# Performance work log

Measured on AMD Instinct MI355X. Metric: run time of the kernel, lower is better.

The kernel has to match this reference:

```python
import jax, jax.numpy as jnp
import numpy as np

B = 65536
R = 160            # radial_len (capped at MAX_RADIAL_LEN)
EDGE_SINK_WIDTH = 8


def setup_inputs() -> dict:
    key = jax.random.key(0)
    k1, k2 = jax.random.split(key)
    return {
        "history": jax.random.uniform(k1, (B, R, 3), dtype=jnp.float32),
        "color_rgb": jax.random.uniform(k2, (B, 3), dtype=jnp.float32),
        "offset_per_frame_60hz": jnp.float32(1.3),
        "persistence_per_frame_60hz": jnp.float32(0.92),
        "diffusion01": jnp.float32(0.5),
        "dt_seconds": jnp.float32(1.0 / 60.0),
        "amount01": jnp.float32(0.8),
        "spread01": jnp.float32(0.4),
    }


def _forward(history, color_rgb, offset, persistence, diffusion01, dt_seconds, amount01, spread01):
    dt = jnp.clip(dt_seconds, 0.0, 0.05)
    dt_scale = dt * 60.0
    dt_offset = offset * dt_scale
    dt_persist = persistence ** dt_scale

    # ---- inject at centre: 5-bin spread kernel, then clamp to [0,1] ----
    amount = jnp.clip(amount01, 0.0, 1.0)
    spread = jnp.clip(spread01, 0.0, 1.0)
    energy = color_rgb * amount                      # [B,3]
    tight = 1.0 - spread
    w = jnp.stack([0.5 + 0.4 * tight,
                   0.2 * spread + 0.05,
                   0.12 * spread,
                   0.06 * spread,
                   0.02 * spread])                   # [5]
    h = history.at[:, :5, :].add(energy[:, None, :] * w[None, :, None])
    h = jnp.clip(h, 0.0, 1.0)

    # ---- semi-Lagrangian push advection (vectorized scatter-add) ----
    i = jnp.arange(R, dtype=h.dtype)                 # source bin positions
    new_pos = i + dt_offset
    valid = (new_pos >= 0.0) & (new_pos < R - 1)     # bins outside are dropped
    left = jnp.clip(jnp.floor(new_pos).astype(jnp.int32), 0, R - 2)
    frac = new_pos - left.astype(h.dtype)
    wl = jnp.where(valid, (1.0 - frac) * dt_persist, 0.0)  # [R]
    wr = jnp.where(valid, frac * dt_persist, 0.0)
    work = jnp.zeros_like(h)
    work = work.at[:, left, :].add(h * wl[None, :, None])
    work = work.at[:, left + 1, :].add(h * wr[None, :, None])
    h = work

    # ---- diffusion: [k, 1-2k, k] stencil with ZERO boundary taps ----
    k = 0.15 * diffusion01
    c = 1.0 - 2.0 * k
    padded = jnp.pad(h, ((0, 0), (1, 1), (0, 0)))    # zero pad matches torch boundary
    h = c * h + k * padded[:, :-2, :] + k * padded[:, 2:, :]

    # ---- quadratic edge sink over last EDGE_SINK_WIDTH bins ----
    idx = jnp.arange(R)
    t = (R - 1 - idx).astype(h.dtype) / float(EDGE_SINK_WIDTH)
    fade = jnp.where(idx >= R - EDGE_SINK_WIDTH, t * t, jnp.ones((), h.dtype))
    h = h * fade[None, :, None]
    return h


def reference(history, color_rgb, offset_per_frame_60hz, persistence_per_frame_60hz,
              diffusion01, dt_seconds, amount01, spread01):
    return _forward(history, color_rgb, offset_per_frame_60hz,
                    persistence_per_frame_60hz, diffusion01, dt_seconds,
                    amount01, spread01)
```

## Files before the change

### kernel.cpp

```cpp
#include <hip/hip_runtime.h>
#include <math.h>

#define RBINS 160
#define BROWS 65536
#define ROWELEMS 480
#define ROWF4 (ROWELEMS / 4)
#define TASKS_PER_ROW 40
#define NTHREADS 256
#define TOTAL_TASKS (BROWS * TASKS_PER_ROW)
#define NBLOCKS (TOTAL_TASKS / NTHREADS)

__device__ __forceinline__ float clamp01(float x) {
    return __builtin_amdgcn_fmed3f(x, 0.0f, 1.0f);
}

template<int P>
__device__ __forceinline__ void stencil_store(
    const float* __restrict__ w,
    float u1, float u2, float u3, float u4,
    float4* __restrict__ dst, bool dofade, int j0)
{
    float r[12];
    #pragma unroll
    for (int m = 0; m < 12; ++m) {
        float acc = u1 * w[P + m];
        acc = fmaf(u2, w[P + m + 3], acc);
        acc = fmaf(u3, w[P + m + 6], acc);
        acc = fmaf(u4, w[P + m + 9], acc);
        r[m] = acc;
    }
    if (dofade) {
        #pragma unroll
        for (int mb = 0; mb < 4; ++mb) {
            const int j = j0 + mb;
            const float t = (float)(RBINS - 1 - j) * 0.125f;
            const float ff = (j >= RBINS - 8) ? t * t : 1.0f;
            r[3*mb+0] *= ff; r[3*mb+1] *= ff; r[3*mb+2] *= ff;
        }
    }
    dst[0] = make_float4(r[0], r[1], r[2],  r[3]);
    dst[1] = make_float4(r[4], r[5], r[6],  r[7]);
    dst[2] = make_float4(r[8], r[9], r[10], r[11]);
}

__global__ __launch_bounds__(NTHREADS, 6) void beat_kernel(
    const float* __restrict__ hist,
    const float* __restrict__ color,
    const float* __restrict__ p_offset,
    const float* __restrict__ p_persist,
    const float* __restrict__ p_diff,
    const float* __restrict__ p_dt,
    const float* __restrict__ p_amount,
    const float* __restrict__ p_spread,
    float* __restrict__ out)
{
    const int task = blockIdx.x * NTHREADS + threadIdx.x;
    const int b = task / TASKS_PER_ROW;
    const int c = task - b * TASKS_PER_ROW;

    const float offs = *p_offset;
    const float pers = *p_persist;
    const float diff = *p_diff;
    const float dts  = *p_dt;

    const float dt       = fminf(fmaxf(dts, 0.0f), 0.05f);
    const float dt_scale = dt * 60.0f;
    const float s        = offs * dt_scale;
    const float dt_pers  = __powf(pers, dt_scale);
    const int   dfl      = (int)floorf(s);
    const float frac     = s - (float)dfl;
    const float kk = 0.15f * diff;
    const float cc = 1.0f - 2.0f * kk;
    const float wl = (1.0f - frac) * dt_pers;
    const float wr = frac * dt_pers;
    const float u1 = wr * kk;
    const float u2 = fmaf(wl, kk, wr * cc);
    const float u3 = fmaf(wl, cc, wr * kk);
    const float u4 = wl * kk;

    const int ilo = max(0, (int)ceilf(-s));
    const int ihi = min(RBINS - 1, (int)ceilf((float)(RBINS - 1) - s) - 1);
    const int flo = 3 * ilo;
    const int fhi = 3 * ihi + 3;

    const int e0 = c * 12;
    const int A  = e0 - 6 - 3 * dfl;
    const int p  = A & 3;
    const int a0 = A - p;

    const float4* src4 = (const float4*)hist + (size_t)b * ROWF4;
    float w[24];
    #pragma unroll
    for (int q = 0; q < 6; ++q) {
        int idx = (a0 >> 2) + q;
        idx = min(max(idx, 0), ROWF4 - 1);
        const float4 v = src4[idx];
        w[4*q+0] = v.x; w[4*q+1] = v.y; w[4*q+2] = v.z; w[4*q+3] = v.w;
    }

    if (a0 < 15) {
        const float am = fminf(fmaxf(*p_amount, 0.0f), 1.0f);
        const float sp = fminf(fmaxf(*p_spread, 0.0f), 1.0f);
        const float tight = 1.0f - sp;
        const float aw0 = am * fmaf(0.4f, tight, 0.5f);
        const float aw1 = am * fmaf(0.2f, sp, 0.05f);
        const float aw2 = am * (0.12f * sp);
        const float aw3 = am * (0.06f * sp);
        const float aw4 = am * (0.02f * sp);
        const float c0 = color[3*b+0];
        const float c1 = color[3*b+1];
        const float c2 = color[3*b+2];
        #pragma unroll
        for (int u = 0; u < 24; ++u) {
            const int f = a0 + u;
            if ((unsigned)f < 15u) {
                const int bin = f / 3;
                const int ch  = f - 3 * bin;
                const float cv = (ch == 0) ? c0 : (ch == 1) ? c1 : c2;
                const float av = (bin == 0) ? aw0 : (bin == 1) ? aw1 :
                                 (bin == 2) ? aw2 : (bin == 3) ? aw3 : aw4;
                w[u] += cv * av;
            }
        }
    }

    #pragma unroll
    for (int u = 0; u < 24; ++u) {
        const int f = a0 + u;
        const bool m = (f >= flo) && (f < fhi);
        w[u] = m ? clamp01(w[u]) : 0.0f;
    }

    float4* dst = (float4*)(out + (size_t)b * ROWELEMS + e0);
    const bool dofade = (c >= TASKS_PER_ROW - 2);
    const int j0 = 4 * c;
    switch (p) {
        case 0:  stencil_store<0>(w, u1, u2, u3, u4, dst, dofade, j0); break;
        case 1:  stencil_store<1>(w, u1, u2, u3, u4, dst, dofade, j0); break;
        case 2:  stencil_store<2>(w, u1, u2, u3, u4, dst, dofade, j0); break;
        default: stencil_store<3>(w, u1, u2, u3, u4, dst, dofade, j0); break;
    }
}

extern "C" void kernel_launch(void* const* d_in, const int* in_sizes, int n_in,
                              void* d_out, int out_size, void* d_ws, size_t ws_size,
                              hipStream_t stream) {
    const float* hist      = (const float*)d_in[0];
    const float* color     = (const float*)d_in[1];
    const float* p_offset  = (const float*)d_in[2];
    const float* p_persist = (const float*)d_in[3];
    const float* p_diff    = (const float*)d_in[4];
    const float* p_dt      = (const float*)d_in[5];
    const float* p_amount  = (const float*)d_in[6];
    const float* p_spread  = (const float*)d_in[7];
    float* outp = (float*)d_out;

    beat_kernel<<<dim3(NBLOCKS), dim3(NTHREADS), 0, stream>>>(
        hist, color, p_offset, p_persist, p_diff, p_dt, p_amount, p_spread, outp);
}
```

Measured before the change: 230.8 us.

## Split inject-region tasks into separate fixup blocks to remove divergent inject path

Main blocks now return early for tasks near the row start that need the centre injection, and 512 extra blocks handle those tasks in a grid-stride loop. This keeps the injection branch and the color loads out of the hot main path, and occupancy bounds are raised from 6 to 8. The cost is extra blocks that partly idle, because fix threads compute but only store when A<15, plus more branching code and register pressure.

```diff
diff --git a/kernel.cpp b/kernel.cpp
--- a/kernel.cpp
+++ b/kernel.cpp
@@ -7,20 +7,22 @@
 #define ROWF4 (ROWELEMS / 4)
 #define TASKS_PER_ROW 40
 #define NTHREADS 256
-#define TOTAL_TASKS (BROWS * TASKS_PER_ROW)
-#define NBLOCKS (TOTAL_TASKS / NTHREADS)
+#define NBLOCKS_MAIN ((BROWS * TASKS_PER_ROW) / NTHREADS)
+#define CFIX 8
+#define NBLOCKS_FIX 512
+#define FIXTHREADS (NBLOCKS_FIX * NTHREADS)
+#define FIXITERS ((BROWS * CFIX) / FIXTHREADS)
 
 __device__ __forceinline__ float clamp01(float x) {
     return __builtin_amdgcn_fmed3f(x, 0.0f, 1.0f);
 }
 
 template<int P>
-__device__ __forceinline__ void stencil_store(
+__device__ __forceinline__ void stencil12(
     const float* __restrict__ w,
     float u1, float u2, float u3, float u4,
-    float4* __restrict__ dst, bool dofade, int j0)
+    float* __restrict__ r)
 {
-    float r[12];
     #pragma unroll
     for (int m = 0; m < 12; ++m) {
         float acc = u1 * w[P + m];
@@ -29,21 +31,31 @@
         acc = fmaf(u4, w[P + m + 9], acc);
         r[m] = acc;
     }
-    if (dofade) {
-        #pragma unroll
-        for (int mb = 0; mb < 4; ++mb) {
-            const int j = j0 + mb;
-            const float t = (float)(RBINS - 1 - j) * 0.125f;
-            const float ff = (j >= RBINS - 8) ? t * t : 1.0f;
-            r[3*mb+0] *= ff; r[3*mb+1] *= ff; r[3*mb+2] *= ff;
+}
+
+__device__ __forceinline__ void inject24(
+    float* __restrict__ w, int a0,
+    const float* __restrict__ color, int b,
+    float aw0, float aw1, float aw2, float aw3, float aw4)
+{
+    const float c0 = color[3*b+0];
+    const float c1 = color[3*b+1];
+    const float c2 = color[3*b+2];
+    #pragma unroll
+    for (int u = 0; u < 24; ++u) {
+        const int f = a0 + u;
+        if ((unsigned)f < 15u) {
+            const int bin = f / 3;
+            const int ch  = f - 3 * bin;
+            const float cv = (ch == 0) ? c0 : (ch == 1) ? c1 : c2;
+            const float av = (bin == 0) ? aw0 : (bin == 1) ? aw1 :
+                             (bin == 2) ? aw2 : (bin == 3) ? aw3 : aw4;
+            w[u] += cv * av;
         }
     }
-    dst[0] = make_float4(r[0], r[1], r[2],  r[3]);
-    dst[1] = make_float4(r[4], r[5], r[6],  r[7]);
-    dst[2] = make_float4(r[8], r[9], r[10], r[11]);
-}
-
-__global__ __launch_bounds__(NTHREADS, 6) void beat_kernel(
+}
+
+__global__ __launch_bounds__(NTHREADS, 8) void beat_kernel(
     const float* __restrict__ hist,
     const float* __restrict__ color,
     const float* __restrict__ p_offset,
@@ -54,10 +66,6 @@
     const float* __restrict__ p_spread,
     float* __restrict__ out)
 {
-    const int task = blockIdx.x * NTHREADS + threadIdx.x;
-    const int b = task / TASKS_PER_ROW;
-    const int c = task - b * TASKS_PER_ROW;
-
     const float offs = *p_offset;
     const float pers = *p_persist;
     const float diff = *p_diff;
@@ -83,22 +91,69 @@
     const int flo = 3 * ilo;
     const int fhi = 3 * ihi + 3;
 
-    const int e0 = c * 12;
-    const int A  = e0 - 6 - 3 * dfl;
-    const int p  = A & 3;
-    const int a0 = A - p;
-
-    const float4* src4 = (const float4*)hist + (size_t)b * ROWF4;
-    float w[24];
-    #pragma unroll
-    for (int q = 0; q < 6; ++q) {
-        int idx = (a0 >> 2) + q;
-        idx = min(max(idx, 0), ROWF4 - 1);
-        const float4 v = src4[idx];
-        w[4*q+0] = v.x; w[4*q+1] = v.y; w[4*q+2] = v.z; w[4*q+3] = v.w;
-    }
-
-    if (a0 < 15) {
+    if (blockIdx.x < NBLOCKS_MAIN) {
+        const int task = blockIdx.x * NTHREADS + threadIdx.x;
+        const int b = task / TASKS_PER_ROW;
+        const int c = task - b * TASKS_PER_ROW;
+        const int e0 = c * 12;
+        const int A  = e0 - 6 - 3 * dfl;
+        const int p  = A & 3;
+        const int a0 = A - p;
+        if (A < 15 && c < CFIX) return;
+
+        const float4* src4 = (const float4*)hist + (size_t)b * ROWF4;
+        float w[24];
+        const int q0 = a0 >> 2;
+        #pragma unroll
+        for (int q = 0; q < 6; ++q) {
+            const int idx = min(max(q0 + q, 0), ROWF4 - 1);
+            const float4 v = src4[idx];
+            w[4*q+0] = v.x; w[4*q+1] = v.y; w[4*q+2] = v.z; w[4*q+3] = v.w;
+        }
+
+        if (A < 15) {
+            const float am = fminf(fmaxf(*p_amount, 0.0f), 1.0f);
+            const float sp = fminf(fmaxf(*p_spread, 0.0f), 1.0f);
+            const float tight = 1.0f - sp;
+            inject24(w, a0, color, b,
+                     am * fmaf(0.4f, tight, 0.5f), am * fmaf(0.2f, sp, 0.05f),
+                     am * (0.12f * sp), am * (0.06f * sp), am * (0.02f * sp));
+        }
+
+        const int lo_u = flo - a0;
+        const int hi_u = fhi - a0;
+        #pragma unroll
+        for (int u = 0; u < 24; ++u) {
+            const bool v = (u >= lo_u) && (u < hi_u);
+            w[u] = v ? clamp01(w[u]) : 0.0f;
+        }
+
+        float r[12];
+        switch (p) {
+            case 0:  stencil12<0>(w, u1, u2, u3, u4, r); break;
+            case 1:  stencil12<1>(w, u1, u2, u3, u4, r); break;
+            case 2:  stencil12<2>(w, u1, u2, u3, u4, r); break;
+            default: stencil12<3>(w, u1, u2, u3, u4, r); break;
+        }
+
+        if (c >= TASKS_PER_ROW - 2) {
+            const int j0 = 4 * c;
+            #pragma unroll
+            for (int mb = 0; mb < 4; ++mb) {
+                const int j = j0 + mb;
+                const float t = (float)(RBINS - 1 - j) * 0.125f;
+                const float ff = (j >= RBINS - 8) ? t * t : 1.0f;
+                r[3*mb+0] *= ff; r[3*mb+1] *= ff; r[3*mb+2] *= ff;
+            }
+        }
+
+        float4* dst = (float4*)(out + (size_t)b * ROWELEMS + e0);
+        dst[0] = make_float4(r[0], r[1], r[2],  r[3]);
+        dst[1] = make_float4(r[4], r[5], r[6],  r[7]);
+        dst[2] = make_float4(r[8], r[9], r[10], r[11]);
+    } else {
+        const int fixtid = (blockIdx.x - NBLOCKS_MAIN) * NTHREADS + threadIdx.x;
+
         const float am = fminf(fmaxf(*p_amount, 0.0f), 1.0f);
         const float sp = fminf(fmaxf(*p_spread, 0.0f), 1.0f);
         const float tight = 1.0f - sp;
@@ -107,38 +162,53 @@
         const float aw2 = am * (0.12f * sp);
         const float aw3 = am * (0.06f * sp);
         const float aw4 = am * (0.02f * sp);
-        const float c0 = color[3*b+0];
-        const float c1 = color[3*b+1];
-        const float c2 = color[3*b+2];
-        #pragma unroll
-        for (int u = 0; u < 24; ++u) {
-            const int f = a0 + u;
-            if ((unsigned)f < 15u) {
-                const int bin = f / 3;
-                const int ch  = f - 3 * bin;
-                const float cv = (ch == 0) ? c0 : (ch == 1) ? c1 : c2;
-                const float av = (bin == 0) ? aw0 : (bin == 1) ? aw1 :
-                                 (bin == 2) ? aw2 : (bin == 3) ? aw3 : aw4;
-                w[u] += cv * av;
-            }
-        }
-    }
-
-    #pragma unroll
-    for (int u = 0; u < 24; ++u) {
-        const int f = a0 + u;
-        const bool m = (f >= flo) && (f < fhi);
-        w[u] = m ? clamp01(w[u]) : 0.0f;
-    }
-
-    float4* dst = (float4*)(out + (size_t)b * ROWELEMS + e0);
-    const bool dofade = (c >= TASKS_PER_ROW - 2);
-    const int j0 = 4 * c;
-    switch (p) {
-        case 0:  stencil_store<0>(w, u1, u2, u3, u4, dst, dofade, j0); break;
-        case 1:  stencil_store<1>(w, u1, u2, u3, u4, dst, dofade, j0); break;
-        case 2:  stencil_store<2>(w, u1, u2, u3, u4, dst, dofade, j0); break;
-        default: stencil_store<3>(w, u1, u2, u3, u4, dst, dofade, j0); break;
+
+        #pragma unroll 1
+        for (int k = 0; k < FIXITERS; ++k) {
+            const int t = fixtid + k * FIXTHREADS;
+            const int b = t >> 3;
+            const int c = t & (CFIX - 1);
+            const int e0 = c * 12;
+            const int A  = e0 - 6 - 3 * dfl;
+            const int p  = A & 3;
+            const int a0 = A - p;
+
+            const float4* src4 = (const float4*)hist + (size_t)b * ROWF4;
+            float w[24];
+            const int q0 = a0 >> 2;
+            #pragma unroll
+            for (int q = 0; q < 6; ++q) {
+                const int idx = min(max(q0 + q, 0), ROWF4 - 1);
+                const float4 v = src4[idx];
+                w[4*q+0] = v.x; w[4*q+1] = v.y; w[4*q+2] = v.z; w[4*q+3] = v.w;
+            }
+
+            if (A < 15)
+                inject24(w, a0, color, b, aw0, aw1, aw2, aw3, aw4);
+
+            const int lo_u = flo - a0;
+            const int hi_u = fhi - a0;
+            #pragma unroll
+            for (int u = 0; u < 24; ++u) {
+                const bool v = (u >= lo_u) && (u < hi_u);
+                w[u] = v ? clamp01(w[u]) : 0.0f;
+            }
+
+            float r[12];
+            switch (p) {
+                case 0:  stencil12<0>(w, u1, u2, u3, u4, r); break;
+                case 1:  stencil12<1>(w, u1, u2, u3, u4, r); break;
+                case 2:  stencil12<2>(w, u1, u2, u3, u4, r); break;
+                default: stencil12<3>(w, u1, u2, u3, u4, r); break;
+            }
+
+            if (A < 15) {
+                float4* dst = (float4*)(out + (size_t)b * ROWELEMS + e0);
+                dst[0] = make_float4(r[0], r[1], r[2],  r[3]);
+                dst[1] = make_float4(r[4], r[5], r[6],  r[7]);
+                dst[2] = make_float4(r[8], r[9], r[10], r[11]);
+            }
+        }
     }
 }
 
@@ -155,6 +225,6 @@
     const float* p_spread  = (const float*)d_in[7];
     float* outp = (float*)d_out;
 
-    beat_kernel<<<dim3(NBLOCKS), dim3(NTHREADS), 0, stream>>>(
+    beat_kernel<<<dim3(NBLOCKS_MAIN + NBLOCKS_FIX), dim3(NTHREADS), 0, stream>>>(
         hist, color, p_offset, p_persist, p_diff, p_dt, p_amount, p_spread, outp);
 }
```

New measurement: 271.4 us. +17.6%, slower.

## Double per-thread output tile, split injection rows into separate fix blocks

Applied to the files above, without the earlier changes.

Each thread now produces 24 output floats (8 bins) instead of 12, loading 9 float4s instead of 6, which cuts the redundant halo loads per output. Threads in the first chunk that need the centre injection return early, and a separate set of blocks handles those rows so the main blocks avoid the divergent injection path. Stores become nontemporal, and the launch bound drops to 4 waves per SIMD to make room for the larger register tile. The risks are lower occupancy and an extra tail of fix blocks.

```diff
diff --git a/kernel.cpp b/kernel.cpp
--- a/kernel.cpp
+++ b/kernel.cpp
@@ -5,45 +5,98 @@
 #define BROWS 65536
 #define ROWELEMS 480
 #define ROWF4 (ROWELEMS / 4)
-#define TASKS_PER_ROW 40
+#define TASKS_PER_ROW 20
 #define NTHREADS 256
-#define TOTAL_TASKS (BROWS * TASKS_PER_ROW)
-#define NBLOCKS (TOTAL_TASKS / NTHREADS)
+#define NBLOCKS_MAIN ((BROWS * TASKS_PER_ROW) / NTHREADS)
+#define NBLOCKS_FIX (BROWS / NTHREADS)
+
+typedef float f32x4 __attribute__((ext_vector_type(4)));
 
 __device__ __forceinline__ float clamp01(float x) {
     return __builtin_amdgcn_fmed3f(x, 0.0f, 1.0f);
 }
 
-template<int P>
-__device__ __forceinline__ void stencil_store(
+__device__ __forceinline__ void nt_store4(float* p, float a, float b, float c, float d) {
+    f32x4 v = {a, b, c, d};
+    __builtin_nontemporal_store(v, (f32x4*)p);
+}
+
+template<int P, int H>
+__device__ __forceinline__ void stencil_half(
     const float* __restrict__ w,
     float u1, float u2, float u3, float u4,
-    float4* __restrict__ dst, bool dofade, int j0)
-{
-    float r[12];
+    float* __restrict__ r)
+{
     #pragma unroll
     for (int m = 0; m < 12; ++m) {
-        float acc = u1 * w[P + m];
-        acc = fmaf(u2, w[P + m + 3], acc);
-        acc = fmaf(u3, w[P + m + 6], acc);
-        acc = fmaf(u4, w[P + m + 9], acc);
+        const int base = P + 12 * H + m;
+        float acc = u1 * w[base];
+        acc = fmaf(u2, w[base + 3], acc);
+        acc = fmaf(u3, w[base + 6], acc);
+        acc = fmaf(u4, w[base + 9], acc);
         r[m] = acc;
     }
-    if (dofade) {
+}
+
+template<int P>
+__device__ __forceinline__ void compute_store24(
+    const float* __restrict__ w,
+    float u1, float u2, float u3, float u4,
+    float* __restrict__ outp, bool fadeq, int bin0)
+{
+    float r[12];
+    stencil_half<P, 0>(w, u1, u2, u3, u4, r);
+    if (fadeq) {
         #pragma unroll
         for (int mb = 0; mb < 4; ++mb) {
-            const int j = j0 + mb;
+            const int j = bin0 + mb;
             const float t = (float)(RBINS - 1 - j) * 0.125f;
             const float ff = (j >= RBINS - 8) ? t * t : 1.0f;
             r[3*mb+0] *= ff; r[3*mb+1] *= ff; r[3*mb+2] *= ff;
         }
     }
-    dst[0] = make_float4(r[0], r[1], r[2],  r[3]);
-    dst[1] = make_float4(r[4], r[5], r[6],  r[7]);
-    dst[2] = make_float4(r[8], r[9], r[10], r[11]);
-}
-
-__global__ __launch_bounds__(NTHREADS, 6) void beat_kernel(
+    nt_store4(outp + 0, r[0], r[1], r[2],  r[3]);
+    nt_store4(outp + 4, r[4], r[5], r[6],  r[7]);
+    nt_store4(outp + 8, r[8], r[9], r[10], r[11]);
+
+    stencil_half<P, 1>(w, u1, u2, u3, u4, r);
+    if (fadeq) {
+        #pragma unroll
+        for (int mb = 0; mb < 4; ++mb) {
+            const int j = bin0 + 4 + mb;
+            const float t = (float)(RBINS - 1 - j) * 0.125f;
+            const float ff = (j >= RBINS - 8) ? t * t : 1.0f;
+            r[3*mb+0] *= ff; r[3*mb+1] *= ff; r[3*mb+2] *= ff;
+        }
+    }
+    nt_store4(outp + 12, r[0], r[1], r[2],  r[3]);
+    nt_store4(outp + 16, r[4], r[5], r[6],  r[7]);
+    nt_store4(outp + 20, r[8], r[9], r[10], r[11]);
+}
+
+__device__ __forceinline__ void inject36(
+    float* __restrict__ w, int a0,
+    const float* __restrict__ color, int b,
+    float aw0, float aw1, float aw2, float aw3, float aw4)
+{
+    const float c0 = color[3*b+0];
+    const float c1 = color[3*b+1];
+    const float c2 = color[3*b+2];
+    #pragma unroll
+    for (int u = 0; u < 36; ++u) {
+        const int f = a0 + u;
+        if ((unsigned)f < 15u) {
+            const int bin = f / 3;
+            const int ch  = f - 3 * bin;
+            const float cv = (ch == 0) ? c0 : (ch == 1) ? c1 : c2;
+            const float av = (bin == 0) ? aw0 : (bin == 1) ? aw1 :
+                             (bin == 2) ? aw2 : (bin == 3) ? aw3 : aw4;
+            w[u] += cv * av;
+        }
+    }
+}
+
+__global__ __launch_bounds__(NTHREADS, 4) void beat_kernel(
     const float* __restrict__ hist,
     const float* __restrict__ color,
     const float* __restrict__ p_offset,
@@ -54,10 +107,6 @@
     const float* __restrict__ p_spread,
     float* __restrict__ out)
 {
-    const int task = blockIdx.x * NTHREADS + threadIdx.x;
-    const int b = task / TASKS_PER_ROW;
-    const int c = task - b * TASKS_PER_ROW;
-
     const float offs = *p_offset;
     const float pers = *p_persist;
     const float diff = *p_diff;
@@ -83,62 +132,78 @@
     const int flo = 3 * ilo;
     const int fhi = 3 * ihi + 3;
 
-    const int e0 = c * 12;
-    const int A  = e0 - 6 - 3 * dfl;
+    int b, c, A;
+    bool is_fix;
+    if (blockIdx.x < NBLOCKS_MAIN) {
+        const int task = blockIdx.x * NTHREADS + threadIdx.x;
+        b = task / TASKS_PER_ROW;
+        c = task - b * TASKS_PER_ROW;
+        A = c * 24 - 6 - 3 * dfl;
+        if (A < 15 && c < 1) return;
+        is_fix = false;
+    } else {
+        b = (blockIdx.x - NBLOCKS_MAIN) * NTHREADS + threadIdx.x;
+        c = 0;
+        A = -6 - 3 * dfl;
+        is_fix = true;
+    }
+
+    const int e0 = c * 24;
     const int p  = A & 3;
     const int a0 = A - p;
+    const int q0 = a0 >> 2;
 
     const float4* src4 = (const float4*)hist + (size_t)b * ROWF4;
-    float w[24];
-    #pragma unroll
-    for (int q = 0; q < 6; ++q) {
-        int idx = (a0 >> 2) + q;
-        idx = min(max(idx, 0), ROWF4 - 1);
-        const float4 v = src4[idx];
-        w[4*q+0] = v.x; w[4*q+1] = v.y; w[4*q+2] = v.z; w[4*q+3] = v.w;
-    }
-
-    if (a0 < 15) {
+    #define CLQ(q) min(max(q0 + (q), 0), ROWF4 - 1)
+    const float4 v0 = src4[CLQ(0)];
+    const float4 v1 = src4[CLQ(1)];
+    const float4 v2 = src4[CLQ(2)];
+    const float4 v3 = src4[CLQ(3)];
+    const float4 v4 = src4[CLQ(4)];
+    const float4 v5 = src4[CLQ(5)];
+    const float4 v6 = src4[CLQ(6)];
+    const float4 v7 = src4[CLQ(7)];
+    const float4 v8 = src4[CLQ(8)];
+    #undef CLQ
+
+    float w[36];
+    w[0]=v0.x; w[1]=v0.y; w[2]=v0.z; w[3]=v0.w;
+    w[4]=v1.x; w[5]=v1.y; w[6]=v1.z; w[7]=v1.w;
+    w[8]=v2.x; w[9]=v2.y; w[10]=v2.z; w[11]=v2.w;
+    w[12]=v3.x; w[13]=v3.y; w[14]=v3.z; w[15]=v3.w;
+    w[16]=v4.x; w[17]=v4.y; w[18]=v4.z; w[19]=v4.w;
+    w[20]=v5.x; w[21]=v5.y; w[22]=v5.z; w[23]=v5.w;
+    w[24]=v6.x; w[25]=v6.y; w[26]=v6.z; w[27]=v6.w;
+    w[28]=v7.x; w[29]=v7.y; w[30]=v7.z; w[31]=v7.w;
+    w[32]=v8.x; w[33]=v8.y; w[34]=v8.z; w[35]=v8.w;
+
+    if (A < 15) {
         const float am = fminf(fmaxf(*p_amount, 0.0f), 1.0f);
         const float sp = fminf(fmaxf(*p_spread, 0.0f), 1.0f);
         const float tight = 1.0f - sp;
-        const float aw0 = am * fmaf(0.4f, tight, 0.5f);
-        const float aw1 = am * fmaf(0.2f, sp, 0.05f);
-        const float aw2 = am * (0.12f * sp);
-        const float aw3 = am * (0.06f * sp);
-        const float aw4 = am * (0.02f * sp);
-        const float c0 = color[3*b+0];
-        const float c1 = color[3*b+1];
-        const float c2 = color[3*b+2];
-        #pragma unroll
-        for (int u = 0; u < 24; ++u) {
-            const int f = a0 + u;
-            if ((unsigned)f < 15u) {
-                const int bin = f / 3;
-                const int ch  = f - 3 * bin;
-                const float cv = (ch == 0) ? c0 : (ch == 1) ? c1 : c2;
-                const float av = (bin == 0) ? aw0 : (bin == 1) ? aw1 :
-                                 (bin == 2) ? aw2 : (bin == 3) ? aw3 : aw4;
-                w[u] += cv * av;
-            }
-        }
-    }
-
+        inject36(w, a0, color, b,
+                 am * fmaf(0.4f, tight, 0.5f), am * fmaf(0.2f, sp, 0.05f),
+                 am * (0.12f * sp), am * (0.06f * sp), am * (0.02f * sp));
+    }
+
+    const int lo_u = flo - a0;
+    const int hi_u = fhi - a0;
     #pragma unroll
-    for (int u = 0; u < 24; ++u) {
-        const int f = a0 + u;
-        const bool m = (f >= flo) && (f < fhi);
-        w[u] = m ? clamp01(w[u]) : 0.0f;
-    }
-
-    float4* dst = (float4*)(out + (size_t)b * ROWELEMS + e0);
-    const bool dofade = (c >= TASKS_PER_ROW - 2);
-    const int j0 = 4 * c;
+    for (int u = 0; u < 36; ++u) {
+        const bool v = (u >= lo_u) && (u < hi_u);
+        w[u] = v ? clamp01(w[u]) : 0.0f;
+    }
+
+    if (is_fix && A >= 15) return;
+
+    float* outp = out + (size_t)b * ROWELEMS + e0;
+    const bool fadeq = (c == TASKS_PER_ROW - 1);
+    const int bin0 = 8 * c;
     switch (p) {
-        case 0:  stencil_store<0>(w, u1, u2, u3, u4, dst, dofade, j0); break;
-        case 1:  stencil_store<1>(w, u1, u2, u3, u4, dst, dofade, j0); break;
-        case 2:  stencil_store<2>(w, u1, u2, u3, u4, dst, dofade, j0); break;
-        default: stencil_store<3>(w, u1, u2, u3, u4, dst, dofade, j0); break;
+        case 0:  compute_store24<0>(w, u1, u2, u3, u4, outp, fadeq, bin0); break;
+        case 1:  compute_store24<1>(w, u1, u2, u3, u4, outp, fadeq, bin0); break;
+        case 2:  compute_store24<2>(w, u1, u2, u3, u4, outp, fadeq, bin0); break;
+        default: compute_store24<3>(w, u1, u2, u3, u4, outp, fadeq, bin0); break;
     }
 }
 
@@ -155,6 +220,6 @@
     const float* p_spread  = (const float*)d_in[7];
     float* outp = (float*)d_out;
 
-    beat_kernel<<<dim3(NBLOCKS), dim3(NTHREADS), 0, stream>>>(
+    beat_kernel<<<dim3(NBLOCKS_MAIN + NBLOCKS_FIX), dim3(NTHREADS), 0, stream>>>(
         hist, color, p_offset, p_persist, p_diff, p_dt, p_amount, p_spread, outp);
 }
```

Result: slower. 422.3 us (+82.9%).

## Process four tasks per thread with software-pipelined loads and split injection path

Applied to the files above, without the earlier changes.

Each thread now handles four 12-float output chunks strided across the grid, double-buffering the six float4 loads so the next chunk's loads are issued before the current chunk's compute, with sched_barriers enforcing that order. The energy injection at the row head moves out of the main blocks into a separate set of fixup blocks that handle the first two chunks of each row, so the main path carries no injection branch. Occupancy drops (launch bounds 6 to 4) to leave room for the extra registers. The goal is better latency hiding on a memory-bound stencil, at the cost of more registers, a larger grid, and more intricate indexing.

```diff
diff --git a/kernel.cpp b/kernel.cpp
--- a/kernel.cpp
+++ b/kernel.cpp
@@ -4,23 +4,69 @@
 #define RBINS 160
 #define BROWS 65536
 #define ROWELEMS 480
-#define ROWF4 (ROWELEMS / 4)
-#define TASKS_PER_ROW 40
+#define ROWF4 120
+#define TPR 40
 #define NTHREADS 256
-#define TOTAL_TASKS (BROWS * TASKS_PER_ROW)
-#define NBLOCKS (TOTAL_TASKS / NTHREADS)
+#define ITERS 4
+#define TOTAL12 (BROWS * TPR)
+#define NBLOCKS_MAIN (TOTAL12 / (NTHREADS * ITERS))
+#define TSTRIDE (NBLOCKS_MAIN * NTHREADS)
+#define NBLOCKS_FIX ((BROWS * 2) / NTHREADS)
 
 __device__ __forceinline__ float clamp01(float x) {
     return __builtin_amdgcn_fmed3f(x, 0.0f, 1.0f);
 }
 
+__device__ __forceinline__ void fill24(
+    float* __restrict__ w,
+    float4 v0, float4 v1, float4 v2, float4 v3, float4 v4, float4 v5)
+{
+    w[0]=v0.x;  w[1]=v0.y;  w[2]=v0.z;  w[3]=v0.w;
+    w[4]=v1.x;  w[5]=v1.y;  w[6]=v1.z;  w[7]=v1.w;
+    w[8]=v2.x;  w[9]=v2.y;  w[10]=v2.z; w[11]=v2.w;
+    w[12]=v3.x; w[13]=v3.y; w[14]=v3.z; w[15]=v3.w;
+    w[16]=v4.x; w[17]=v4.y; w[18]=v4.z; w[19]=v4.w;
+    w[20]=v5.x; w[21]=v5.y; w[22]=v5.z; w[23]=v5.w;
+}
+
+__device__ __forceinline__ void maskclamp24(
+    float* __restrict__ w, int lo_u, int hi_u)
+{
+    #pragma unroll
+    for (int u = 0; u < 24; ++u) {
+        const bool v = (u >= lo_u) && (u < hi_u);
+        w[u] = v ? clamp01(w[u]) : 0.0f;
+    }
+}
+
+__device__ __forceinline__ void inject24w(
+    float* __restrict__ w, int a0,
+    const float* __restrict__ color, int b,
+    float aw0, float aw1, float aw2, float aw3, float aw4)
+{
+    const float c0 = color[3*b+0];
+    const float c1 = color[3*b+1];
+    const float c2 = color[3*b+2];
+    #pragma unroll
+    for (int u = 0; u < 24; ++u) {
+        const int f = a0 + u;
+        if ((unsigned)f < 15u) {
+            const int bin = f / 3;
+            const int ch  = f - 3 * bin;
+            const float cv = (ch == 0) ? c0 : (ch == 1) ? c1 : c2;
+            const float av = (bin == 0) ? aw0 : (bin == 1) ? aw1 :
+                             (bin == 2) ? aw2 : (bin == 3) ? aw3 : aw4;
+            w[u] += cv * av;
+        }
+    }
+}
+
 template<int P>
-__device__ __forceinline__ void stencil_store(
+__device__ __forceinline__ void stencil12(
     const float* __restrict__ w,
     float u1, float u2, float u3, float u4,
-    float4* __restrict__ dst, bool dofade, int j0)
-{
-    float r[12];
+    float* __restrict__ r)
+{
     #pragma unroll
     for (int m = 0; m < 12; ++m) {
         float acc = u1 * w[P + m];
@@ -29,21 +75,130 @@
         acc = fmaf(u4, w[P + m + 9], acc);
         r[m] = acc;
     }
-    if (dofade) {
+}
+
+__device__ __forceinline__ void loads6(
+    const float* __restrict__ hist, int b, int q0,
+    float4& v0, float4& v1, float4& v2, float4& v3, float4& v4, float4& v5)
+{
+    const float4* s = (const float4*)hist + (size_t)b * ROWF4;
+    v0 = s[min(max(q0 + 0, 0), ROWF4 - 1)];
+    v1 = s[min(max(q0 + 1, 0), ROWF4 - 1)];
+    v2 = s[min(max(q0 + 2, 0), ROWF4 - 1)];
+    v3 = s[min(max(q0 + 3, 0), ROWF4 - 1)];
+    v4 = s[min(max(q0 + 4, 0), ROWF4 - 1)];
+    v5 = s[min(max(q0 + 5, 0), ROWF4 - 1)];
+}
+
+template<int P>
+__device__ __forceinline__ void comp12(
+    float4 v0, float4 v1, float4 v2, float4 v3, float4 v4, float4 v5,
+    int lo_u, int hi_u,
+    float u1, float u2, float u3, float u4,
+    bool doinj, int a0, const float* __restrict__ color, int b,
+    float aw0, float aw1, float aw2, float aw3, float aw4,
+    bool dostore, bool fadeq, int bin0, float* __restrict__ outp)
+{
+    float w[24];
+    fill24(w, v0, v1, v2, v3, v4, v5);
+    if (doinj) inject24w(w, a0, color, b, aw0, aw1, aw2, aw3, aw4);
+    maskclamp24(w, lo_u, hi_u);
+    float r[12];
+    stencil12<P>(w, u1, u2, u3, u4, r);
+    if (fadeq) {
         #pragma unroll
         for (int mb = 0; mb < 4; ++mb) {
-            const int j = j0 + mb;
+            const int j = bin0 + mb;
             const float t = (float)(RBINS - 1 - j) * 0.125f;
             const float ff = (j >= RBINS - 8) ? t * t : 1.0f;
             r[3*mb+0] *= ff; r[3*mb+1] *= ff; r[3*mb+2] *= ff;
         }
     }
-    dst[0] = make_float4(r[0], r[1], r[2],  r[3]);
-    dst[1] = make_float4(r[4], r[5], r[6],  r[7]);
-    dst[2] = make_float4(r[8], r[9], r[10], r[11]);
-}
-
-__global__ __launch_bounds__(NTHREADS, 6) void beat_kernel(
+    if (dostore) {
+        *(float4*)(outp + 0) = make_float4(r[0], r[1], r[2],  r[3]);
+        *(float4*)(outp + 4) = make_float4(r[4], r[5], r[6],  r[7]);
+        *(float4*)(outp + 8) = make_float4(r[8], r[9], r[10], r[11]);
+    }
+}
+
+__device__ __forceinline__ void geo(
+    int t, int K, int flo, int fhi,
+    int& b, int& c, int& q0, int& a0, int& lo, int& hi)
+{
+    b  = t / TPR;
+    c  = t - b * TPR;
+    q0 = 3 * c - K;
+    a0 = 4 * q0;
+    lo = flo - a0;
+    hi = fhi - a0;
+}
+
+template<int P>
+__device__ __forceinline__ void mainbody(
+    int t0, const float* __restrict__ hist, const float* __restrict__ color,
+    float* __restrict__ out, int K, int flo, int fhi,
+    float u1, float u2, float u3, float u4,
+    float aw0, float aw1, float aw2, float aw3, float aw4)
+{
+    int bA, cA, qA, aA, loA, hiA;
+    int bB, cB, qB, aB, loB, hiB;
+    float4 x0, x1, x2, x3, x4, x5;
+    float4 y0, y1, y2, y3, y4, y5;
+
+    geo(t0, K, flo, fhi, bA, cA, qA, aA, loA, hiA);
+    loads6(hist, bA, qA, x0, x1, x2, x3, x4, x5);
+
+    geo(t0 + TSTRIDE, K, flo, fhi, bB, cB, qB, aB, loB, hiB);
+    loads6(hist, bB, qB, y0, y1, y2, y3, y4, y5);
+    __builtin_amdgcn_sched_barrier(0);
+    {
+        const int Af = aA + P;
+        const bool inj = (Af < 15) && (cA >= 2);
+        const bool dst = !((Af < 15) && (cA < 2));
+        comp12<P>(x0, x1, x2, x3, x4, x5, loA, hiA, u1, u2, u3, u4,
+                  inj, aA, color, bA, aw0, aw1, aw2, aw3, aw4,
+                  dst, cA >= 38, 4 * cA,
+                  out + (size_t)bA * ROWELEMS + 12 * cA);
+    }
+
+    geo(t0 + 2 * TSTRIDE, K, flo, fhi, bA, cA, qA, aA, loA, hiA);
+    loads6(hist, bA, qA, x0, x1, x2, x3, x4, x5);
+    __builtin_amdgcn_sched_barrier(0);
+    {
+        const int Af = aB + P;
+        const bool inj = (Af < 15) && (cB >= 2);
+        const bool dst = !((Af < 15) && (cB < 2));
+        comp12<P>(y0, y1, y2, y3, y4, y5, loB, hiB, u1, u2, u3, u4,
+                  inj, aB, color, bB, aw0, aw1, aw2, aw3, aw4,
+                  dst, cB >= 38, 4 * cB,
+                  out + (size_t)bB * ROWELEMS + 12 * cB);
+    }
+
+    geo(t0 + 3 * TSTRIDE, K, flo, fhi, bB, cB, qB, aB, loB, hiB);
+    loads6(hist, bB, qB, y0, y1, y2, y3, y4, y5);
+    __builtin_amdgcn_sched_barrier(0);
+    {
+        const int Af = aA + P;
+        const bool inj = (Af < 15) && (cA >= 2);
+        const bool dst = !((Af < 15) && (cA < 2));
+        comp12<P>(x0, x1, x2, x3, x4, x5, loA, hiA, u1, u2, u3, u4,
+                  inj, aA, color, bA, aw0, aw1, aw2, aw3, aw4,
+                  dst, cA >= 38, 4 * cA,
+                  out + (size_t)bA * ROWELEMS + 12 * cA);
+    }
+
+    {
+        const int Af = aB + P;
+        const bool inj = (Af < 15) && (cB >= 2);
+        const bool dst = !((Af < 15) && (cB < 2));
+        comp12<P>(y0, y1, y2, y3, y4, y5, loB, hiB, u1, u2, u3, u4,
+                  inj, aB, color, bB, aw0, aw1, aw2, aw3, aw4,
+                  dst, cB >= 38, 4 * cB,
+                  out + (size_t)bB * ROWELEMS + 12 * cB);
+    }
+}
+
+__global__ __launch_bounds__(NTHREADS, 4) void beat_kernel(
     const float* __restrict__ hist,
     const float* __restrict__ color,
     const float* __restrict__ p_offset,
@@ -54,10 +209,6 @@
     const float* __restrict__ p_spread,
     float* __restrict__ out)
 {
-    const int task = blockIdx.x * NTHREADS + threadIdx.x;
-    const int b = task / TASKS_PER_ROW;
-    const int c = task - b * TASKS_PER_ROW;
-
     const float offs = *p_offset;
     const float pers = *p_persist;
     const float diff = *p_diff;
@@ -83,62 +234,56 @@
     const int flo = 3 * ilo;
     const int fhi = 3 * ihi + 3;
 
-    const int e0 = c * 12;
-    const int A  = e0 - 6 - 3 * dfl;
-    const int p  = A & 3;
-    const int a0 = A - p;
-
-    const float4* src4 = (const float4*)hist + (size_t)b * ROWF4;
-    float w[24];
-    #pragma unroll
-    for (int q = 0; q < 6; ++q) {
-        int idx = (a0 >> 2) + q;
-        idx = min(max(idx, 0), ROWF4 - 1);
-        const float4 v = src4[idx];
-        w[4*q+0] = v.x; w[4*q+1] = v.y; w[4*q+2] = v.z; w[4*q+3] = v.w;
-    }
-
-    if (a0 < 15) {
-        const float am = fminf(fmaxf(*p_amount, 0.0f), 1.0f);
-        const float sp = fminf(fmaxf(*p_spread, 0.0f), 1.0f);
-        const float tight = 1.0f - sp;
-        const float aw0 = am * fmaf(0.4f, tight, 0.5f);
-        const float aw1 = am * fmaf(0.2f, sp, 0.05f);
-        const float aw2 = am * (0.12f * sp);
-        const float aw3 = am * (0.06f * sp);
-        const float aw4 = am * (0.02f * sp);
-        const float c0 = color[3*b+0];
-        const float c1 = color[3*b+1];
-        const float c2 = color[3*b+2];
-        #pragma unroll
-        for (int u = 0; u < 24; ++u) {
-            const int f = a0 + u;
-            if ((unsigned)f < 15u) {
-                const int bin = f / 3;
-                const int ch  = f - 3 * bin;
-                const float cv = (ch == 0) ? c0 : (ch == 1) ? c1 : c2;
-                const float av = (bin == 0) ? aw0 : (bin == 1) ? aw1 :
-                                 (bin == 2) ? aw2 : (bin == 3) ? aw3 : aw4;
-                w[u] += cv * av;
-            }
+    const int S = 6 + 3 * dfl;
+    const int p = (-S) & 3;
+    const int K = (S + p) >> 2;
+
+    const float am = fminf(fmaxf(*p_amount, 0.0f), 1.0f);
+    const float sp = fminf(fmaxf(*p_spread, 0.0f), 1.0f);
+    const float tight = 1.0f - sp;
+    const float aw0 = am * fmaf(0.4f, tight, 0.5f);
+    const float aw1 = am * fmaf(0.2f, sp, 0.05f);
+    const float aw2 = am * (0.12f * sp);
+    const float aw3 = am * (0.06f * sp);
+    const float aw4 = am * (0.02f * sp);
+
+    if (blockIdx.x < NBLOCKS_MAIN) {
+        const int t0 = blockIdx.x * NTHREADS + threadIdx.x;
+        switch (p) {
+            case 0:  mainbody<0>(t0, hist, color, out, K, flo, fhi,
+                                 u1,u2,u3,u4, aw0,aw1,aw2,aw3,aw4); break;
+            case 1:  mainbody<1>(t0, hist, color, out, K, flo, fhi,
+                                 u1,u2,u3,u4, aw0,aw1,aw2,aw3,aw4); break;
+            case 2:  mainbody<2>(t0, hist, color, out, K, flo, fhi,
+                                 u1,u2,u3,u4, aw0,aw1,aw2,aw3,aw4); break;
+            default: mainbody<3>(t0, hist, color, out, K, flo, fhi,
+                                 u1,u2,u3,u4, aw0,aw1,aw2,aw3,aw4); break;
         }
-    }
-
-    #pragma unroll
-    for (int u = 0; u < 24; ++u) {
-        const int f = a0 + u;
-        const bool m = (f >= flo) && (f < fhi);
-        w[u] = m ? clamp01(w[u]) : 0.0f;
-    }
-
-    float4* dst = (float4*)(out + (size_t)b * ROWELEMS + e0);
-    const bool dofade = (c >= TASKS_PER_ROW - 2);
-    const int j0 = 4 * c;
-    switch (p) {
-        case 0:  stencil_store<0>(w, u1, u2, u3, u4, dst, dofade, j0); break;
-        case 1:  stencil_store<1>(w, u1, u2, u3, u4, dst, dofade, j0); break;
-        case 2:  stencil_store<2>(w, u1, u2, u3, u4, dst, dofade, j0); break;
-        default: stencil_store<3>(w, u1, u2, u3, u4, dst, dofade, j0); break;
+    } else {
+        const int t = (blockIdx.x - NBLOCKS_MAIN) * NTHREADS + threadIdx.x;
+        const int b = t >> 1;
+        const int c = t & 1;
+        const int A = 12 * c - S;
+        if (A >= 15) return;
+        int bb, cc2, q0, a0, lo, hi;
+        geo(b * TPR + c, K, flo, fhi, bb, cc2, q0, a0, lo, hi);
+        float4 v0, v1, v2, v3, v4, v5;
+        loads6(hist, b, q0, v0, v1, v2, v3, v4, v5);
+        float* outp = out + (size_t)b * ROWELEMS + 12 * c;
+        switch (p) {
+            case 0:  comp12<0>(v0,v1,v2,v3,v4,v5, lo, hi, u1,u2,u3,u4,
+                               true, a0, color, b, aw0,aw1,aw2,aw3,aw4,
+                               true, false, 4*c, outp); break;
+            case 1:  comp12<1>(v0,v1,v2,v3,v4,v5, lo, hi, u1,u2,u3,u4,
+                               true, a0, color, b, aw0,aw1,aw2,aw3,aw4,
+                               true, false, 4*c, outp); break;
+            case 2:  comp12<2>(v0,v1,v2,v3,v4,v5, lo, hi, u1,u2,u3,u4,
+                               true, a0, color, b, aw0,aw1,aw2,aw3,aw4,
+                               true, false, 4*c, outp); break;
+            default: comp12<3>(v0,v1,v2,v3,v4,v5, lo, hi, u1,u2,u3,u4,
+                               true, a0, color, b, aw0,aw1,aw2,aw3,aw4,
+                               true, false, 4*c, outp); break;
+        }
     }
 }
 
@@ -155,6 +300,6 @@
     const float* p_spread  = (const float*)d_in[7];
     float* outp = (float*)d_out;
 
-    beat_kernel<<<dim3(NBLOCKS), dim3(NTHREADS), 0, stream>>>(
+    beat_kernel<<<dim3(NBLOCKS_MAIN + NBLOCKS_FIX), dim3(NTHREADS), 0, stream>>>(
         hist, color, p_offset, p_persist, p_diff, p_dt, p_amount, p_spread, outp);
 }
```

Measured after the change: 254.1 us. 10.1% more time.
